# Kernel optimization log

Hardware: AMD Instinct MI355X
Metric: run time of the kernel (lower is better)

Reference implementation:

```python
import jax, jax.numpy as jnp
import numpy as np

BN_EPS = 1e-5

def _conv(x, w, pad):
    return jax.lax.conv_general_dilated(
        x, w, window_strides=(1, 1), padding=[(pad, pad), (pad, pad)],
        dimension_numbers=('NCHW', 'OIHW', 'NCHW'))

def setup_inputs() -> dict:
    key = jax.random.key(0)
    ks = jax.random.split(key, 6)
    B, C1, C2, H, W, k = 4, 128, 256, 64, 64, 3
    N = k * k
    x = jax.random.normal(ks[0], (B, C1, H, W), jnp.float32)
    pw_w = jax.random.normal(ks[1], (C2, C1, 1, 1), jnp.float32) * 0.05
    bn_gamma = jnp.ones((C2,), jnp.float32)
    bn_beta = jnp.zeros((C2,), jnp.float32)
    bn_mean = jax.random.normal(ks[2], (C2,), jnp.float32) * 0.1
    bn_var = jax.random.uniform(ks[3], (C2,), jnp.float32, minval=0.5, maxval=1.5)
    off_w = jax.random.normal(ks[4], (2 * N, C2, 3, 3), jnp.float32) * 0.01
    off_b = jnp.zeros((2 * N,), jnp.float32)
    dcn_w = jax.random.normal(ks[5], (C2, C2, k, k), jnp.float32) * 0.02
    return dict(x=x, pw_w=pw_w, bn_gamma=bn_gamma, bn_beta=bn_beta,
                bn_mean=bn_mean, bn_var=bn_var, off_w=off_w, off_b=off_b,
                dcn_w=dcn_w)

def reference(x, pw_w, bn_gamma, bn_beta, bn_mean, bn_var, off_w, off_b, dcn_w):
    B, C1, H, W = x.shape
    C2 = pw_w.shape[0]
    k = dcn_w.shape[-1]
    N = k * k
    # ---- 1x1 pointwise conv + BatchNorm (eval mode), act=False ----
    xp = _conv(x, pw_w, 0)
    scale = bn_gamma * jax.lax.rsqrt(bn_var + BN_EPS)
    xp = xp * scale[None, :, None, None] + (bn_beta - bn_mean * scale)[None, :, None, None]
    # ---- offset prediction conv: [B, 2N, H, W]; first N = dy, last N = dx ----
    offset = _conv(xp, off_w, 1) + off_b[None, :, None, None]
    off_y, off_x = offset[:, :N], offset[:, N:]
    # ---- sampling positions p = p0 + p_n + offset ----
    gy, gx = jnp.meshgrid(jnp.arange(H, dtype=jnp.float32),
                          jnp.arange(W, dtype=jnp.float32), indexing='ij')
    kk = jnp.arange(k, dtype=jnp.float32) - (k // 2)
    ky, kx = jnp.meshgrid(kk, kk, indexing='ij')
    py = gy[None, None] + ky.reshape(N)[None, :, None, None] + off_y  # [B,N,H,W]
    px = gx[None, None] + kx.reshape(N)[None, :, None, None] + off_x
    py = jnp.clip(py, 0.0, H - 1.0)
    px = jnp.clip(px, 0.0, W - 1.0)

    def sample_one(img, py_b, px_b):  # img [C2,H,W], py/px [N,H,W]
        y0 = jnp.floor(py_b)
        x0 = jnp.floor(px_b)
        wy = py_b - y0
        wx = px_b - x0
        y0i = y0.astype(jnp.int32)
        x0i = x0.astype(jnp.int32)
        y1i = jnp.minimum(y0i + 1, H - 1)
        x1i = jnp.minimum(x0i + 1, W - 1)
        flat = img.reshape(C2, H * W)
        def g(yy, xx):
            idx = (yy * W + xx).reshape(-1)
            return flat[:, idx].reshape(C2, N, H, W)
        v00 = g(y0i, x0i); v01 = g(y0i, x1i)
        v10 = g(y1i, x0i); v11 = g(y1i, x1i)
        wy = wy[None]; wx = wx[None]
        return (v00 * (1 - wy) * (1 - wx) + v01 * (1 - wy) * wx +
                v10 * wy * (1 - wx) + v11 * wy * wx)

    sampled = jax.vmap(sample_one)(xp, py, px)  # [B,C2,N,H,W]
    # ---- deformable conv = weighted sum over kernel points ----
    out = jnp.einsum('bcnhw,ocn->bohw', sampled, dcn_w.reshape(C2, C2, N))
    return jax.nn.silu(out)
```

## Files before the change

kernel.cpp:

```cpp
#include <hip/hip_runtime.h>
#include <math.h>

#define XP_F   0
#define OFF_F  4194304
#define XPH_F  4489216
#define WTB_F  6586368
#define PART_F 6881280

typedef short bf16x8 __attribute__((ext_vector_type(8)));
typedef float f32x4 __attribute__((ext_vector_type(4)));

__device__ inline unsigned short f2b(float f) {
    union { float f; unsigned u; } v; v.f = f;
    unsigned r = v.u + 0x7FFF + ((v.u >> 16) & 1);
    return (unsigned short)(r >> 16);
}
__device__ inline float b2f(unsigned short h) {
    union { unsigned u; float f; } v; v.u = ((unsigned)h) << 16; return v.f;
}

__global__ __launch_bounds__(256) void k0_prep(const float* __restrict__ dcn,
                                               unsigned short* __restrict__ wTb) {
    int idx = blockIdx.x * 256 + threadIdx.x;
    int n = idx >> 16, o = (idx >> 8) & 255, c = idx & 255;
    wTb[idx] = f2b(dcn[(o * 256 + c) * 9 + n]);
}

__global__ __launch_bounds__(256, 4) void k1_pw_bn(const float* __restrict__ x,
                                                   const float* __restrict__ pw,
                                                   const float* __restrict__ gamma,
                                                   const float* __restrict__ beta,
                                                   const float* __restrict__ mean,
                                                   const float* __restrict__ var,
                                                   float* __restrict__ xp,
                                                   unsigned short* __restrict__ xph) {
    __shared__ float wl[128 * 64];
    int t = threadIdx.x;
    int m0 = blockIdx.x * 64;
    int b = m0 >> 12;
    int hw = (m0 & 4095) + (t & 63);
    int q = t >> 6;
    int c2base = blockIdx.y * 64;

    for (int i = 0; i < 32; ++i) {
        int idx = t + 256 * i;
        int kk = idx >> 6, c2l = idx & 63;
        wl[idx] = pw[(c2base + c2l) * 128 + kk];
    }
    __syncthreads();

    float acc[16];
#pragma unroll
    for (int i = 0; i < 16; ++i) acc[i] = 0.f;

    const float* xb = x + (b * 128) * 4096 + hw;
    for (int kk = 0; kk < 128; kk += 8) {
        float xv[8];
#pragma unroll
        for (int u = 0; u < 8; ++u) xv[u] = xb[(kk + u) * 4096];
#pragma unroll
        for (int u = 0; u < 8; ++u) {
            const float4* w4 = (const float4*)&wl[(kk + u) * 64 + q * 16];
#pragma unroll
            for (int i = 0; i < 4; ++i) {
                float4 wv = w4[i];
                acc[i * 4 + 0] += xv[u] * wv.x;
                acc[i * 4 + 1] += xv[u] * wv.y;
                acc[i * 4 + 2] += xv[u] * wv.z;
                acc[i * 4 + 3] += xv[u] * wv.w;
            }
        }
    }
    bf16x8 r0, r1;
#pragma unroll
    for (int i = 0; i < 16; ++i) {
        int c2 = c2base + q * 16 + i;
        float s = gamma[c2] * rsqrtf(var[c2] + 1e-5f);
        float v = acc[i] * s + (beta[c2] - mean[c2] * s);
        xp[((b * 256 + c2) << 12) + hw] = v;
        if (i < 8) r0[i] = (short)f2b(v); else r1[i - 8] = (short)f2b(v);
    }
    unsigned short* hb = xph + (((b << 12) + hw) << 8) + c2base + q * 16;
    *(bf16x8*)hb = r0;
    *(bf16x8*)(hb + 8) = r1;
}

__global__ __launch_bounds__(256) void k2a_off(const float* __restrict__ xp,
                                               const float* __restrict__ offw,
                                               float* __restrict__ part) {
    __shared__ float xl[3 * 32 * 66];
    __shared__ float wl[9 * 18 * 32];
    int t = threadIdx.x;
    int bx = blockIdx.x;
    int b = bx >> 9, h = (bx >> 3) & 63, cs = bx & 7;
    int w = t & 63, jset = t >> 6;
    const int jbase_a[4] = {0, 5, 10, 14};
    const int jcnt_a[4] = {5, 5, 4, 4};
    int jbase = jbase_a[jset], jcnt = jcnt_a[jset];
    float acc[5] = {0.f, 0.f, 0.f, 0.f, 0.f};
    int cbase = cs * 32;

    for (int idx = t; idx < 3 * 32 * 66; idx += 256) {
        int dy = idx / 2112, rem = idx % 2112;
        int c = rem / 66, col = rem % 66;
        int y = h + dy - 1, wc = col - 1;
        float v = 0.f;
        if ((unsigned)y < 64u && (unsigned)wc < 64u)
            v = xp[((b * 256 + cbase + c) << 12) + y * 64 + wc];
        xl[idx] = v;
    }
    for (int idx = t; idx < 18 * 32 * 9; idx += 256) {
        int j = idx / 288, c = (idx / 9) % 32, tap = idx % 9;
        wl[(tap * 18 + j) * 32 + c] = offw[(j * 256 + cbase + c) * 9 + tap];
    }
    __syncthreads();
#pragma unroll
    for (int tap = 0; tap < 9; ++tap) {
        int dy = tap / 3, dx = tap % 3;
        const float* xrow = &xl[dy * 2112 + (w + dx)];
        const float4* wrow = (const float4*)&wl[(tap * 18 + jbase) * 32];
#pragma unroll
        for (int c4 = 0; c4 < 8; ++c4) {
            float xv0 = xrow[(c4 * 4 + 0) * 66];
            float xv1 = xrow[(c4 * 4 + 1) * 66];
            float xv2 = xrow[(c4 * 4 + 2) * 66];
            float xv3 = xrow[(c4 * 4 + 3) * 66];
#pragma unroll
            for (int jj = 0; jj < 5; ++jj) {
                if (jj < jcnt) {
                    float4 wv = wrow[jj * 8 + c4];
                    acc[jj] += xv0 * wv.x + xv1 * wv.y + xv2 * wv.z + xv3 * wv.w;
                }
            }
        }
    }
    for (int jj = 0; jj < 5; ++jj) {
        if (jj < jcnt)
            part[(((cs * 4 + b) * 18 + jbase + jj) << 12) + h * 64 + w] = acc[jj];
    }
}

__global__ __launch_bounds__(256) void k2b_red(const float* __restrict__ part,
                                               const float* __restrict__ offb,
                                               float* __restrict__ off) {
    int i = blockIdx.x * 256 + threadIdx.x;
    int j = (i >> 12) % 18;
    float s = offb[j];
#pragma unroll
    for (int cs = 0; cs < 8; ++cs) s += part[cs * 294912 + i];
    off[i] = s;
}

__global__ __launch_bounds__(512, 4) void k3_dcn(const unsigned short* __restrict__ xph,
                                                 const float* __restrict__ off,
                                                 const unsigned short* __restrict__ wTb,
                                                 float* __restrict__ out) {
    __shared__ int   i00[288], i01[288], i10[288], i11[288];
    __shared__ float w00[288], w01[288], w10[288], w11[288];
    __shared__ unsigned short smp[2][16 * 64 * 8];

    int t = threadIdx.x;
    int orig = blockIdx.x;
    int bx = (orig & 7) * 64 + (orig >> 3);
    int b = bx >> 7, h = (bx >> 1) & 63, wh = (bx & 1) * 32;
    int wv = t >> 6, l = t & 63;
    const unsigned short* xb = xph + (b << 20);

    if (t < 288) {
        int n = t >> 5, p = t & 31;
        int w = wh + p;
        float oy = off[((b * 18 + n) << 12) + h * 64 + w];
        float ox = off[((b * 18 + n + 9) << 12) + h * 64 + w];
        float py = (float)(h + n / 3 - 1) + oy;
        float px = (float)(w + n % 3 - 1) + ox;
        py = fminf(fmaxf(py, 0.f), 63.f);
        px = fminf(fmaxf(px, 0.f), 63.f);
        float fy = floorf(py), fx = floorf(px);
        int y0 = (int)fy, x0 = (int)fx;
        float wy = py - fy, wx = px - fx;
        int y1 = min(y0 + 1, 63), x1 = min(x0 + 1, 63);
        i00[t] = (y0 * 64 + x0) << 8;  i01[t] = (y0 * 64 + x1) << 8;
        i10[t] = (y1 * 64 + x0) << 8;  i11[t] = (y1 * 64 + x1) << 8;
        w00[t] = (1.f - wy) * (1.f - wx);  w01[t] = (1.f - wy) * wx;
        w10[t] = wy * (1.f - wx);          w11[t] = wy * wx;
    }
    __syncthreads();

    int pt_p = wv & 1;
    int ks0 = wv >> 1;
    int px_p = pt_p * 16 + (l & 15);
    int cgl = l >> 4;

    bf16x8 g[2][4];

    auto stage_issue = [&](int tap) {
        int sb = tap * 32 + px_p;
        int a00 = i00[sb], a01 = i01[sb], a10 = i10[sb], a11 = i11[sb];
#pragma unroll
        for (int ku = 0; ku < 2; ++ku) {
            int ks = ks0 + ku * 4;
            int c = (ks * 4 + cgl) << 3;
            g[ku][0] = *(const bf16x8*)(xb + a00 + c);
            g[ku][1] = *(const bf16x8*)(xb + a01 + c);
            g[ku][2] = *(const bf16x8*)(xb + a10 + c);
            g[ku][3] = *(const bf16x8*)(xb + a11 + c);
        }
    };
    auto stage_write = [&](int tap) {
        int bu = tap & 1;
        int sb = tap * 32 + px_p;
        float b00 = w00[sb], b01 = w01[sb], b10 = w10[sb], b11 = w11[sb];
#pragma unroll
        for (int ku = 0; ku < 2; ++ku) {
            bf16x8 r;
#pragma unroll
            for (int j = 0; j < 8; ++j) {
                float v = b00 * b2f((unsigned short)g[ku][0][j]) +
                          b01 * b2f((unsigned short)g[ku][1][j]) +
                          b10 * b2f((unsigned short)g[ku][2][j]) +
                          b11 * b2f((unsigned short)g[ku][3][j]);
                r[j] = (short)f2b(v);
            }
            int F = pt_p * 8 + ks0 + ku * 4;
            *(bf16x8*)&smp[bu][(F * 64 + (l ^ (F & 7))) << 3] = r;
        }
    };

    stage_issue(0);
    __builtin_amdgcn_sched_barrier(0);
    stage_write(0);
    __syncthreads();

    f32x4 acc[2][2];
#pragma unroll
    for (int i = 0; i < 2; ++i)
#pragma unroll
        for (int j = 0; j < 2; ++j) acc[i][j] = (f32x4)0.f;

    int arow = l & 15, areg = l >> 4;
    for (int tap = 0; tap < 9; ++tap) {
        if (tap < 8) stage_issue(tap + 1);
        __builtin_amdgcn_sched_barrier(0);
        int bu = tap & 1;
        const unsigned short* wbase =
            wTb + (tap * 256 + wv * 32 + arow) * 256 + areg * 8;
        __builtin_amdgcn_s_setprio(1);
#pragma unroll
        for (int ks = 0; ks < 8; ++ks) {
            bf16x8 a0 = *(const bf16x8*)(wbase + ks * 32);
            bf16x8 a1 = *(const bf16x8*)(wbase + 16 * 256 + ks * 32);
#pragma unroll
            for (int pt = 0; pt < 2; ++pt) {
                int F = pt * 8 + ks;
                bf16x8 bfr = *(const bf16x8*)
                    &smp[bu][(F * 64 + (l ^ (F & 7))) << 3];
                acc[0][pt] = __builtin_amdgcn_mfma_f32_16x16x32_bf16(a0, bfr, acc[0][pt], 0, 0, 0);
                acc[1][pt] = __builtin_amdgcn_mfma_f32_16x16x32_bf16(a1, bfr, acc[1][pt], 0, 0, 0);
            }
        }
        __builtin_amdgcn_s_setprio(0);
        __builtin_amdgcn_sched_barrier(0);
        if (tap < 8) stage_write(tap + 1);
        __syncthreads();
    }

#pragma unroll
    for (int ot = 0; ot < 2; ++ot)
#pragma unroll
        for (int pt = 0; pt < 2; ++pt) {
            int px = wh + pt * 16 + (l & 15);
#pragma unroll
            for (int j = 0; j < 4; ++j) {
                int o = wv * 32 + ot * 16 + (l >> 4) * 4 + j;
                float a = acc[ot][pt][j];
                out[((b * 256 + o) << 12) + h * 64 + px] = a / (1.f + expf(-a));
            }
        }
}

extern "C" void kernel_launch(void* const* d_in, const int* in_sizes, int n_in,
                              void* d_out, int out_size, void* d_ws, size_t ws_size,
                              hipStream_t stream) {
    const float* x     = (const float*)d_in[0];
    const float* pw    = (const float*)d_in[1];
    const float* gamma = (const float*)d_in[2];
    const float* beta  = (const float*)d_in[3];
    const float* mean  = (const float*)d_in[4];
    const float* var   = (const float*)d_in[5];
    const float* offw  = (const float*)d_in[6];
    const float* offb  = (const float*)d_in[7];
    const float* dcn   = (const float*)d_in[8];
    float* ws = (float*)d_ws;
    float* xp   = ws + XP_F;
    float* off  = ws + OFF_F;
    unsigned short* xph = (unsigned short*)(ws + XPH_F);
    unsigned short* wTb = (unsigned short*)(ws + WTB_F);
    float* part = ws + PART_F;
    float* out = (float*)d_out;

    hipLaunchKernelGGL(k0_prep, dim3(2304), dim3(256), 0, stream, dcn, wTb);
    hipLaunchKernelGGL(k1_pw_bn, dim3(256, 4), dim3(256), 0, stream,
                       x, pw, gamma, beta, mean, var, xp, xph);
    hipLaunchKernelGGL(k2a_off, dim3(2048), dim3(256), 0, stream, xp, offw, part);
    hipLaunchKernelGGL(k2b_red, dim3(1152), dim3(256), 0, stream, part, offb, off);
    hipLaunchKernelGGL(k3_dcn, dim3(512), dim3(512), 0, stream, xph, off, wTb, out);
}
```

Baseline: 285.2 us.

## Split deformable conv into separate bilinear sampling and MFMA GEMM kernels

Splits the fused deformable-conv kernel into two. The first materializes the bilinearly sampled bf16 tiles for every tap to a workspace buffer, in a swizzled layout. The second streams those tiles into LDS with global_load_lds double-buffering and runs the MFMA GEMM plus SiLU. The aim is to take the irregular gather and interpolation math off the GEMM's critical path, at the cost of an extra round trip through global memory (about 37 MB written and read) and an added launch. The fused path is kept as a fallback when the workspace is too small.

```diff
diff --git a/kernel.cpp b/kernel.cpp
--- a/kernel.cpp
+++ b/kernel.cpp
@@ -6,6 +6,8 @@
 #define XPH_F  4489216
 #define WTB_F  6586368
 #define PART_F 6881280
+#define SAMP_F 9240576
+#define SPLIT_END_F 28114944ULL
 
 typedef short bf16x8 __attribute__((ext_vector_type(8)));
 typedef float f32x4 __attribute__((ext_vector_type(4)));
@@ -151,6 +153,138 @@
     off[i] = s;
 }
 
+__global__ __launch_bounds__(256) void k3a_samp(const unsigned short* __restrict__ xph,
+                                                const float* __restrict__ off,
+                                                unsigned short* __restrict__ samp) {
+    __shared__ int   c00[32], c01[32], c10[32], c11[32];
+    __shared__ float4 wts[32];
+    int t = threadIdx.x;
+    int bid = blockIdx.x;
+    int b = bid / 1152, r = bid % 1152;
+    int tap = r >> 7, pb = r & 127;
+    int h = pb >> 1, wh = (pb & 1) * 32;
+
+    if (t < 32) {
+        int w = wh + t;
+        int hw = h * 64 + w;
+        float oy = off[((b * 18 + tap) << 12) + hw];
+        float ox = off[((b * 18 + tap + 9) << 12) + hw];
+        float py = (float)(h + tap / 3 - 1) + oy;
+        float px = (float)(w + tap % 3 - 1) + ox;
+        py = fminf(fmaxf(py, 0.f), 63.f);
+        px = fminf(fmaxf(px, 0.f), 63.f);
+        float fy = floorf(py), fx = floorf(px);
+        int y0 = (int)fy, x0 = (int)fx;
+        float wy = py - fy, wx = px - fx;
+        int y1 = min(y0 + 1, 63), x1 = min(x0 + 1, 63);
+        c00[t] = (y0 * 64 + x0) << 8;  c01[t] = (y0 * 64 + x1) << 8;
+        c10[t] = (y1 * 64 + x0) << 8;  c11[t] = (y1 * 64 + x1) << 8;
+        wts[t] = make_float4((1.f - wy) * (1.f - wx), (1.f - wy) * wx,
+                             wy * (1.f - wx), wy * wx);
+    }
+    __syncthreads();
+
+    const unsigned short* xb = xph + (b << 20);
+    unsigned short* sb = samp + bid * 8192;
+#pragma unroll
+    for (int i = 0; i < 4; ++i) {
+        int u = i * 256 + t;
+        int F = u >> 6, chunk = u & 63;
+        int lane = chunk ^ (F & 7);
+        int pxl = (F >> 3) * 16 + (lane & 15);
+        int co = ((F & 7) * 4 + (lane >> 4)) << 3;
+        float4 wv = wts[pxl];
+        bf16x8 v00 = *(const bf16x8*)(xb + c00[pxl] + co);
+        bf16x8 v01 = *(const bf16x8*)(xb + c01[pxl] + co);
+        bf16x8 v10 = *(const bf16x8*)(xb + c10[pxl] + co);
+        bf16x8 v11 = *(const bf16x8*)(xb + c11[pxl] + co);
+        bf16x8 rr;
+#pragma unroll
+        for (int j = 0; j < 8; ++j) {
+            float v = wv.x * b2f((unsigned short)v00[j]) +
+                      wv.y * b2f((unsigned short)v01[j]) +
+                      wv.z * b2f((unsigned short)v10[j]) +
+                      wv.w * b2f((unsigned short)v11[j]);
+            rr[j] = (short)f2b(v);
+        }
+        *(bf16x8*)(sb + (u << 3)) = rr;
+    }
+}
+
+__global__ __launch_bounds__(512, 4) void k3b_gemm(const unsigned short* __restrict__ samp,
+                                                   const unsigned short* __restrict__ wTb,
+                                                   float* __restrict__ out) {
+    __shared__ unsigned short smp[2][8192];
+    int t = threadIdx.x;
+    int orig = blockIdx.x;
+    int bx = (orig & 7) * 64 + (orig >> 3);
+    int b = bx >> 7, h = (bx >> 1) & 63, half = bx & 1, wh = half * 32;
+    int wv = t >> 6, l = t & 63;
+    int tile0 = (b * 9) * 128 + h * 2 + half;
+
+    auto stage = [&](int tap) {
+        const unsigned short* src = samp + (tile0 + tap * 128) * 8192 + t * 8;
+        unsigned short* dst = &smp[tap & 1][t * 8];
+#if __has_builtin(__builtin_amdgcn_global_load_lds)
+        __builtin_amdgcn_global_load_lds(
+            (const __attribute__((address_space(1))) unsigned int*)src,
+            (__attribute__((address_space(3))) unsigned int*)dst, 16, 0, 0);
+        __builtin_amdgcn_global_load_lds(
+            (const __attribute__((address_space(1))) unsigned int*)(src + 4096),
+            (__attribute__((address_space(3))) unsigned int*)(dst + 4096), 16, 0, 0);
+#else
+        *(bf16x8*)dst = *(const bf16x8*)src;
+        *(bf16x8*)(dst + 4096) = *(const bf16x8*)(src + 4096);
+#endif
+    };
+
+    stage(0);
+    __syncthreads();
+
+    f32x4 acc[2][2];
+#pragma unroll
+    for (int i = 0; i < 2; ++i)
+#pragma unroll
+        for (int j = 0; j < 2; ++j) acc[i][j] = (f32x4)0.f;
+
+    int arow = l & 15, areg = l >> 4;
+    for (int tap = 0; tap < 9; ++tap) {
+        if (tap < 8) stage(tap + 1);
+        int bu = tap & 1;
+        const unsigned short* wbase =
+            wTb + (tap * 256 + wv * 32 + arow) * 256 + areg * 8;
+        __builtin_amdgcn_s_setprio(1);
+#pragma unroll
+        for (int ks = 0; ks < 8; ++ks) {
+            bf16x8 a0 = *(const bf16x8*)(wbase + ks * 32);
+            bf16x8 a1 = *(const bf16x8*)(wbase + 16 * 256 + ks * 32);
+#pragma unroll
+            for (int pt = 0; pt < 2; ++pt) {
+                int F = pt * 8 + ks;
+                bf16x8 bfr = *(const bf16x8*)
+                    &smp[bu][(F * 64 + (l ^ (F & 7))) << 3];
+                acc[0][pt] = __builtin_amdgcn_mfma_f32_16x16x32_bf16(a0, bfr, acc[0][pt], 0, 0, 0);
+                acc[1][pt] = __builtin_amdgcn_mfma_f32_16x16x32_bf16(a1, bfr, acc[1][pt], 0, 0, 0);
+            }
+        }
+        __builtin_amdgcn_s_setprio(0);
+        __syncthreads();
+    }
+
+#pragma unroll
+    for (int ot = 0; ot < 2; ++ot)
+#pragma unroll
+        for (int pt = 0; pt < 2; ++pt) {
+            int px = wh + pt * 16 + (l & 15);
+#pragma unroll
+            for (int j = 0; j < 4; ++j) {
+                int o = wv * 32 + ot * 16 + (l >> 4) * 4 + j;
+                float a = acc[ot][pt][j];
+                out[((b * 256 + o) << 12) + h * 64 + px] = a / (1.f + expf(-a));
+            }
+        }
+}
+
 __global__ __launch_bounds__(512, 4) void k3_dcn(const unsigned short* __restrict__ xph,
                                                  const float* __restrict__ off,
                                                  const unsigned short* __restrict__ wTb,
@@ -158,7 +292,6 @@
     __shared__ int   i00[288], i01[288], i10[288], i11[288];
     __shared__ float w00[288], w01[288], w10[288], w11[288];
     __shared__ unsigned short smp[2][16 * 64 * 8];
-
     int t = threadIdx.x;
     int orig = blockIdx.x;
     int bx = (orig & 7) * 64 + (orig >> 3);
@@ -190,7 +323,6 @@
     int ks0 = wv >> 1;
     int px_p = pt_p * 16 + (l & 15);
     int cgl = l >> 4;
-
     bf16x8 g[2][4];
 
     auto stage_issue = [&](int tap) {
@@ -296,6 +428,7 @@
     unsigned short* xph = (unsigned short*)(ws + XPH_F);
     unsigned short* wTb = (unsigned short*)(ws + WTB_F);
     float* part = ws + PART_F;
+    unsigned short* samp = (unsigned short*)(ws + SAMP_F);
     float* out = (float*)d_out;
 
     hipLaunchKernelGGL(k0_prep, dim3(2304), dim3(256), 0, stream, dcn, wTb);
@@ -303,5 +436,10 @@
                        x, pw, gamma, beta, mean, var, xp, xph);
     hipLaunchKernelGGL(k2a_off, dim3(2048), dim3(256), 0, stream, xp, offw, part);
     hipLaunchKernelGGL(k2b_red, dim3(1152), dim3(256), 0, stream, part, offb, off);
-    hipLaunchKernelGGL(k3_dcn, dim3(512), dim3(512), 0, stream, xph, off, wTb, out);
-}
+    if (ws_size >= SPLIT_END_F * 4ULL) {
+        hipLaunchKernelGGL(k3a_samp, dim3(4608), dim3(256), 0, stream, xph, off, samp);
+        hipLaunchKernelGGL(k3b_gemm, dim3(512), dim3(512), 0, stream, samp, wTb, out);
+    } else {
+        hipLaunchKernelGGL(k3_dcn, dim3(512), dim3(512), 0, stream, xph, off, wTb, out);
+    }
+}
```

After: 289.3 us. About the same (+1.5%).
